# Kernel optimization log

Hardware: AMD Instinct MI355X
Metric: run time of the kernel (lower is better)

Reference implementation:

```python
import jax, jax.numpy as jnp
import numpy as np


def group_norm(x, gamma, beta, groups, eps=1e-5):
    B, C, H, W = x.shape
    xg = x.reshape(B, groups, C // groups, H, W)
    mu = xg.mean(axis=(2, 3, 4), keepdims=True)
    var = xg.var(axis=(2, 3, 4), keepdims=True)
    xn = ((xg - mu) * jax.lax.rsqrt(var + eps)).reshape(B, C, H, W)
    return xn * gamma[:, None, None] + beta[:, None, None]


def setup_inputs() -> dict:
    key = jax.random.key(0)
    ks = jax.random.split(key, 8)
    B, C, H, W = 4, 32, 256, 256
    return {
        "dec4": jax.random.normal(ks[0], (B, 512, 16, 16), jnp.float32),
        "feat": jax.random.normal(ks[1], (B, 64, H, W), jnp.float32),
        "gn_pre_gamma": jnp.ones((64,), jnp.float32),
        "gn_pre_beta": jnp.zeros((64,), jnp.float32),
        "W_pre": jax.random.normal(ks[2], (8, 64), jnp.float32) * 0.05,
        "b_pre": jnp.zeros((8,), jnp.float32),
        "gn_gap_gamma": jnp.ones((512,), jnp.float32),
        "gn_gap_beta": jnp.zeros((512,), jnp.float32),
        "W_gap": jax.random.normal(ks[3], (256, 512), jnp.float32) * 0.05,
        "b_gap": jnp.zeros((256,), jnp.float32),
        "emb": jax.random.normal(ks[4], (C, 256), jnp.float32),
        "W_ctrl": jax.random.normal(ks[5], (153, 512), jnp.float32) * 0.05,
        "b_ctrl": jnp.zeros((153,), jnp.float32),
    }


def reference(dec4, feat, gn_pre_gamma, gn_pre_beta, W_pre, b_pre,
              gn_gap_gamma, gn_gap_beta, W_gap, b_gap, emb, W_ctrl, b_ctrl):
    B = feat.shape[0]
    C = emb.shape[0]  # number of classes / dynamic-head instances
    # precls_conv: GroupNorm(16,64) -> ReLU -> 1x1 conv 64->8
    pre = jax.nn.relu(group_norm(feat, gn_pre_gamma, gn_pre_beta, 16))
    head_in = jnp.einsum('oi,bihw->bohw', W_pre, pre) + b_pre[:, None, None]  # [B,8,H,W]
    # GAP branch: GroupNorm(16,512) -> ReLU -> global avg pool -> 1x1 conv 512->256
    g = jax.nn.relu(group_norm(dec4, gn_gap_gamma, gn_gap_beta, 16)).mean(axis=(2, 3))  # [B,512]
    x_feat = g @ W_gap.T + b_gap  # [B,256]
    # controller: per (batch, class) dynamic conv params (1x1 conv == linear)
    x_cond = jnp.concatenate([
        jnp.broadcast_to(x_feat[:, None, :], (B, C, 256)),
        jnp.broadcast_to(emb[None], (B, C, 256)),
    ], axis=-1)  # [B,C,512]
    params = x_cond @ W_ctrl.T + b_ctrl  # [B,C,153]
    # split per weight_nums=[64,64,8], bias_nums=[8,8,1]
    w1 = params[..., 0:64].reshape(B, C, 8, 8)    # [out=8, in=8]
    w2 = params[..., 64:128].reshape(B, C, 8, 8)
    w3 = params[..., 128:136]                     # [out=1, in=8]
    b1 = params[..., 136:144]
    b2 = params[..., 144:152]
    b3 = params[..., 152:153]
    # batched grouped 1x1 convs (one group per (batch,class) instance)
    x1 = jax.nn.relu(jnp.einsum('bcoi,bihw->bcohw', w1, head_in) + b1[..., None, None])
    x2 = jax.nn.relu(jnp.einsum('bcoi,bcihw->bcohw', w2, x1) + b2[..., None, None])
    logits = jnp.einsum('bci,bcihw->bchw', w3, x2) + b3[..., None]  # [B,C,H,W]
    return logits
```

## Files before the change

### kernel.cpp

```cpp
#include <hip/hip_runtime.h>
#include <hip/hip_fp16.h>

typedef __fp16 h2 __attribute__((ext_vector_type(2)));

#if defined(__has_builtin)
#if __has_builtin(__builtin_amdgcn_fdot2)
#define HAVE_FDOT2 1
#endif
#endif

__device__ inline float dot2f(h2 a, h2 b, float acc) {
#ifdef HAVE_FDOT2
    return __builtin_amdgcn_fdot2(a, b, acc, false);
#else
    return acc + (float)a.x * (float)b.x + (float)a.y * (float)b.y;
#endif
}

__device__ inline float wave_sum(float v) {
#pragma unroll
    for (int off = 32; off > 0; off >>= 1) v += __shfl_down(v, off, 64);
    return v;
}

__global__ __launch_bounds__(256) void prep(
    const float* __restrict__ feat, const float* __restrict__ dec4,
    const float* __restrict__ gn_gap_gamma, const float* __restrict__ gn_gap_beta,
    const float* __restrict__ emb, const float* __restrict__ W_ctrl,
    float* __restrict__ partials, float* __restrict__ g_buf,
    float* __restrict__ E_ws) {
    int blk = blockIdx.x;
    int tid = threadIdx.x;
    int wid = tid >> 6, lane = tid & 63;
    if (blk < 512) {
        int grp = blk >> 3;
        int chunk = blk & 7;
        const float4* base = (const float4*)(feat + (size_t)grp * 262144 + (size_t)chunk * 32768);
        float sa = 0.f, qa = 0.f, sb = 0.f, qb = 0.f;
#pragma unroll 8
        for (int i = 0; i < 16; ++i) {
            float4 v = base[i * 256 + tid];
            float4 u = base[(i + 16) * 256 + tid];
            sa += v.x + v.y + v.z + v.w;
            qa += v.x * v.x + v.y * v.y + v.z * v.z + v.w * v.w;
            sb += u.x + u.y + u.z + u.w;
            qb += u.x * u.x + u.y * u.y + u.z * u.z + u.w * u.w;
        }
        __shared__ float ls[4], lq[4];
        float s = wave_sum(sa + sb);
        float q = wave_sum(qa + qb);
        if (lane == 0) { ls[wid] = s; lq[wid] = q; }
        __syncthreads();
        if (tid == 0) {
            partials[blk * 2 + 0] = ls[0] + ls[1] + ls[2] + ls[3];
            partials[blk * 2 + 1] = lq[0] + lq[1] + lq[2] + lq[3];
        }
    } else if (blk < 576) {
        int idx = blk - 512;
        int b = idx >> 4, gi = idx & 15;
        const float* base = dec4 + (size_t)idx * 8192;
        int ch = tid >> 3, sub = tid & 7;
        const float4* r = (const float4*)(base + ch * 256 + sub * 32);
        float v[32];
        float s = 0.f, q = 0.f;
#pragma unroll
        for (int i = 0; i < 8; ++i) {
            float4 a = r[i];
            v[i * 4 + 0] = a.x; v[i * 4 + 1] = a.y; v[i * 4 + 2] = a.z; v[i * 4 + 3] = a.w;
            s += a.x + a.y + a.z + a.w;
            q += a.x * a.x + a.y * a.y + a.z * a.z + a.w * a.w;
        }
        __shared__ float ls[4], lq[4], bc[2];
        s = wave_sum(s); q = wave_sum(q);
        if (lane == 0) { ls[wid] = s; lq[wid] = q; }
        __syncthreads();
        if (tid == 0) {
            float S = ls[0] + ls[1] + ls[2] + ls[3];
            float Q = lq[0] + lq[1] + lq[2] + lq[3];
            const float inv = 1.f / 8192.f;
            float mu = S * inv;
            float var = Q * inv - mu * mu;
            bc[0] = mu;
            bc[1] = rsqrtf(var + 1e-5f);
        }
        __syncthreads();
        float mu = bc[0], rs = bc[1];
        int c = gi * 32 + ch;
        float sc = rs * gn_gap_gamma[c];
        float sh = gn_gap_beta[c] - mu * sc;
        float acc = 0.f;
#pragma unroll
        for (int i = 0; i < 32; ++i) acc += fmaxf(v[i] * sc + sh, 0.f);
#pragma unroll
        for (int m = 1; m < 8; m <<= 1) acc += __shfl_xor(acc, m, 64);
        if (sub == 0) g_buf[b * 512 + c] = acc * (1.f / 256.f);
    } else {
        int c = blk - 576;
        __shared__ float es[256];
        es[tid] = emb[c * 256 + tid];
        __syncthreads();
        if (tid < 153) {
            const float4* w4 = (const float4*)(W_ctrl + tid * 512 + 256);
            const float4* e4 = (const float4*)es;
            float acc = 0.f;
#pragma unroll 8
            for (int k = 0; k < 64; ++k) {
                float4 a = w4[k], e = e4[k];
                acc += a.x * e.x + a.y * e.y + a.z * e.z + a.w * e.w;
            }
            E_ws[c * 153 + tid] = acc;
        }
    }
}

__global__ __launch_bounds__(256) void fc(
    const float* __restrict__ g_buf, const float* __restrict__ W_gap,
    const float* __restrict__ b_gap, const float* __restrict__ W_ctrl,
    const float* __restrict__ b_ctrl, const float* __restrict__ E_ws,
    unsigned char* __restrict__ pk) {
    int b = blockIdx.x, tid = threadIdx.x;
    __shared__ float gs[512];
    __shared__ float xf[256];
    __shared__ float F[160];
    gs[tid] = g_buf[b * 512 + tid];
    gs[tid + 256] = g_buf[b * 512 + 256 + tid];
    __syncthreads();
    {
        const float4* w = (const float4*)(W_gap + tid * 512);
        const float4* g4 = (const float4*)gs;
        float acc = b_gap[tid];
#pragma unroll 8
        for (int k = 0; k < 128; ++k) {
            float4 wv = w[k], gv = g4[k];
            acc += wv.x * gv.x + wv.y * gv.y + wv.z * gv.z + wv.w * gv.w;
        }
        xf[tid] = acc;
    }
    __syncthreads();
    if (tid < 160) {
        float acc = 0.f;
        if (tid < 153) {
            const float4* w = (const float4*)(W_ctrl + tid * 512);
            const float4* x4 = (const float4*)xf;
#pragma unroll 8
            for (int k = 0; k < 64; ++k) {
                float4 wv = w[k], xv = x4[k];
                acc += wv.x * xv.x + wv.y * xv.y + wv.z * xv.z + wv.w * xv.w;
            }
            acc += b_ctrl[tid];
        }
        F[tid] = acc;
    }
    __syncthreads();
    unsigned char* dst = pk + (size_t)b * 10240;
    for (int c = 0; c < 32; ++c) {
        if (tid < 152) {
            float v = F[tid] + E_ws[c * 153 + tid];
            ((__fp16*)(dst + c * 320))[tid] = (__fp16)v;
        } else if (tid == 152) {
            *(float*)(dst + c * 320 + 304) = F[152] + E_ws[c * 153 + 152];
        }
    }
}

__global__ __launch_bounds__(512, 4) void mainK(
    const float* __restrict__ feat, const float* __restrict__ partials,
    const float* __restrict__ gamma, const float* __restrict__ beta,
    const float* __restrict__ W_pre, const float* __restrict__ b_pre,
    const float4* __restrict__ pk, float* __restrict__ out) {
    int blk = blockIdx.x;
    int b = blk >> 7;
    int tid = threadIdx.x;
    int w = tid >> 6, lane = tid & 63;
    int P0 = (blk & 127) << 9;

    __shared__ __align__(16) float smem[4768];
    float4* pp   = (float4*)smem;
    float4* hi_l = (float4*)(smem + 2560);
    float* scv = smem + 4608;
    float* shv = smem + 4672;
    float* mus = smem + 4736;
    float* rss = smem + 4752;

    const float4* src = pk + (size_t)b * 640;
    for (int i = tid; i < 640; i += 512) pp[i] = src[i];

    if (tid < 16) {
        float s = 0.f, q = 0.f;
#pragma unroll
        for (int cc = 0; cc < 8; ++cc) {
            int idx = ((b * 16 + tid) * 8 + cc) * 2;
            s += partials[idx]; q += partials[idx + 1];
        }
        const float inv = 1.f / 262144.f;
        float mu = s * inv;
        float var = q * inv - mu * mu;
        mus[tid] = mu; rss[tid] = rsqrtf(var + 1e-5f);
    }
    __syncthreads();
    if (tid < 64) {
        float mu = mus[tid >> 2], rs = rss[tid >> 2];
        float sg = rs * gamma[tid];
        scv[tid] = sg;
        shv[tid] = beta[tid] - mu * sg;
    }
    __syncthreads();

    {
        float hi[8];
#pragma unroll
        for (int o = 0; o < 8; ++o) hi[o] = b_pre[o];
        const float* fb = feat + ((size_t)b << 22) + P0 + tid;
#pragma unroll
        for (int ch = 0; ch < 64; ++ch) {
            float v = fb[(size_t)ch << 16];
            float pre = fmaxf(v * scv[ch] + shv[ch], 0.f);
#pragma unroll
            for (int o = 0; o < 8; ++o) hi[o] += W_pre[o * 64 + ch] * pre;
        }
        float4 hq;
        hq.x = __builtin_bit_cast(float, __builtin_amdgcn_cvt_pkrtz(hi[0], hi[1]));
        hq.y = __builtin_bit_cast(float, __builtin_amdgcn_cvt_pkrtz(hi[2], hi[3]));
        hq.z = __builtin_bit_cast(float, __builtin_amdgcn_cvt_pkrtz(hi[4], hi[5]));
        hq.w = __builtin_bit_cast(float, __builtin_amdgcn_cvt_pkrtz(hi[6], hi[7]));
        hi_l[(tid >> 1) + (tid & 1) * 256] = hq;
    }
    __syncthreads();

    float* ob = out + ((size_t)b << 21) + P0;
#pragma unroll 1
    for (int kk = 0; kk < 4; ++kk) {
        int c = (w << 2) + kk;
        const float4* Pc = pp + c * 20;
        float4 w1r[8], w2r[8];
#pragma unroll
        for (int o = 0; o < 8; ++o) w1r[o] = Pc[o];
#pragma unroll
        for (int o = 0; o < 8; ++o) w2r[o] = Pc[8 + o];
        float4 w3r = Pc[16];
        float4 b1r = Pc[17];
        float4 b2r = Pc[18];
        float b3v = Pc[19].x;
        float b1f[8], b2f[8];
        { h2 t = __builtin_bit_cast(h2, b1r.x); b1f[0] = t.x; b1f[1] = t.y; }
        { h2 t = __builtin_bit_cast(h2, b1r.y); b1f[2] = t.x; b1f[3] = t.y; }
        { h2 t = __builtin_bit_cast(h2, b1r.z); b1f[4] = t.x; b1f[5] = t.y; }
        { h2 t = __builtin_bit_cast(h2, b1r.w); b1f[6] = t.x; b1f[7] = t.y; }
        { h2 t = __builtin_bit_cast(h2, b2r.x); b2f[0] = t.x; b2f[1] = t.y; }
        { h2 t = __builtin_bit_cast(h2, b2r.y); b2f[2] = t.x; b2f[3] = t.y; }
        { h2 t = __builtin_bit_cast(h2, b2r.z); b2f[4] = t.x; b2f[5] = t.y; }
        { h2 t = __builtin_bit_cast(h2, b2r.w); b2f[6] = t.x; b2f[7] = t.y; }

        float* cp = ob + ((size_t)c << 16);
#pragma unroll
        for (int j = 0; j < 4; ++j) {
            int q = j * 64 + lane;
            float4 ha = hi_l[q];
            float4 hb = hi_l[256 + q];
            h2 a0 = __builtin_bit_cast(h2, ha.x), a1 = __builtin_bit_cast(h2, ha.y),
               a2 = __builtin_bit_cast(h2, ha.z), a3 = __builtin_bit_cast(h2, ha.w);
            h2 e0 = __builtin_bit_cast(h2, hb.x), e1 = __builtin_bit_cast(h2, hb.y),
               e2 = __builtin_bit_cast(h2, hb.z), e3 = __builtin_bit_cast(h2, hb.w);

            float x1a[8], x1b[8];
#pragma unroll
            for (int o = 0; o < 8; ++o) {
                h2 wa = __builtin_bit_cast(h2, w1r[o].x), wb = __builtin_bit_cast(h2, w1r[o].y),
                   wc = __builtin_bit_cast(h2, w1r[o].z), wd = __builtin_bit_cast(h2, w1r[o].w);
                float s0 = dot2f(wd, a3, dot2f(wc, a2, dot2f(wb, a1, dot2f(wa, a0, b1f[o]))));
                float s1 = dot2f(wd, e3, dot2f(wc, e2, dot2f(wb, e1, dot2f(wa, e0, b1f[o]))));
                x1a[o] = fmaxf(s0, 0.f);
                x1b[o] = fmaxf(s1, 0.f);
            }
            h2 pa0 = __builtin_amdgcn_cvt_pkrtz(x1a[0], x1a[1]);
            h2 pa1 = __builtin_amdgcn_cvt_pkrtz(x1a[2], x1a[3]);
            h2 pa2 = __builtin_amdgcn_cvt_pkrtz(x1a[4], x1a[5]);
            h2 pa3 = __builtin_amdgcn_cvt_pkrtz(x1a[6], x1a[7]);
            h2 pb0 = __builtin_amdgcn_cvt_pkrtz(x1b[0], x1b[1]);
            h2 pb1 = __builtin_amdgcn_cvt_pkrtz(x1b[2], x1b[3]);
            h2 pb2 = __builtin_amdgcn_cvt_pkrtz(x1b[4], x1b[5]);
            h2 pb3 = __builtin_amdgcn_cvt_pkrtz(x1b[6], x1b[7]);

            float x2a[8], x2b[8];
#pragma unroll
            for (int o = 0; o < 8; ++o) {
                h2 wa = __builtin_bit_cast(h2, w2r[o].x), wb = __builtin_bit_cast(h2, w2r[o].y),
                   wc = __builtin_bit_cast(h2, w2r[o].z), wd = __builtin_bit_cast(h2, w2r[o].w);
                float s0 = dot2f(wd, pa3, dot2f(wc, pa2, dot2f(wb, pa1, dot2f(wa, pa0, b2f[o]))));
                float s1 = dot2f(wd, pb3, dot2f(wc, pb2, dot2f(wb, pb1, dot2f(wa, pb0, b2f[o]))));
                x2a[o] = fmaxf(s0, 0.f);
                x2b[o] = fmaxf(s1, 0.f);
            }
            h2 qa0 = __builtin_amdgcn_cvt_pkrtz(x2a[0], x2a[1]);
            h2 qa1 = __builtin_amdgcn_cvt_pkrtz(x2a[2], x2a[3]);
            h2 qa2 = __builtin_amdgcn_cvt_pkrtz(x2a[4], x2a[5]);
            h2 qa3 = __builtin_amdgcn_cvt_pkrtz(x2a[6], x2a[7]);
            h2 qb0 = __builtin_amdgcn_cvt_pkrtz(x2b[0], x2b[1]);
            h2 qb1 = __builtin_amdgcn_cvt_pkrtz(x2b[2], x2b[3]);
            h2 qb2 = __builtin_amdgcn_cvt_pkrtz(x2b[4], x2b[5]);
            h2 qb3 = __builtin_amdgcn_cvt_pkrtz(x2b[6], x2b[7]);

            h2 w3a = __builtin_bit_cast(h2, w3r.x), w3b = __builtin_bit_cast(h2, w3r.y),
               w3c = __builtin_bit_cast(h2, w3r.z), w3d = __builtin_bit_cast(h2, w3r.w);
            float lg0 = dot2f(w3d, qa3, dot2f(w3c, qa2, dot2f(w3b, qa1, dot2f(w3a, qa0, b3v))));
            float lg1 = dot2f(w3d, qb3, dot2f(w3c, qb2, dot2f(w3b, qb1, dot2f(w3a, qb0, b3v))));
            *(float2*)(cp + 2 * q) = make_float2(lg0, lg1);
        }
    }
}

extern "C" void kernel_launch(void* const* d_in, const int* in_sizes, int n_in,
                              void* d_out, int out_size, void* d_ws, size_t ws_size,
                              hipStream_t stream) {
    const float* dec4         = (const float*)d_in[0];
    const float* feat         = (const float*)d_in[1];
    const float* gn_pre_gamma = (const float*)d_in[2];
    const float* gn_pre_beta  = (const float*)d_in[3];
    const float* W_pre        = (const float*)d_in[4];
    const float* b_pre        = (const float*)d_in[5];
    const float* gn_gap_gamma = (const float*)d_in[6];
    const float* gn_gap_beta  = (const float*)d_in[7];
    const float* W_gap        = (const float*)d_in[8];
    const float* b_gap        = (const float*)d_in[9];
    const float* emb          = (const float*)d_in[10];
    const float* W_ctrl       = (const float*)d_in[11];
    const float* b_ctrl       = (const float*)d_in[12];
    float* out = (float*)d_out;
    float* ws  = (float*)d_ws;

    float* partials = ws;
    float* g_buf    = ws + 1024;
    float* E_ws     = ws + 3072;
    unsigned char* pkB = (unsigned char*)(ws + 7968);

    prep<<<608, 256, 0, stream>>>(feat, dec4, gn_gap_gamma, gn_gap_beta,
                                  emb, W_ctrl, partials, g_buf, E_ws);
    fc<<<4, 256, 0, stream>>>(g_buf, W_gap, b_gap, W_ctrl, b_ctrl, E_ws, pkB);
    mainK<<<512, 512, 0, stream>>>(feat, partials, gn_pre_gamma, gn_pre_beta,
                                   W_pre, b_pre, (const float4*)pkB, out);
}
```

Before: 90.82 us.

## Split feat stats into more blocks and vectorize dynamic-head output stores

The GroupNorm statistics pass over feat is split into 2048 smaller blocks instead of 512, giving more parallelism for the memory-bound reduction. The main kernel reorders the fp16 head_in tile in shared memory so each lane handles four consecutive pixels and writes a float4 instead of a float2. It also packs the scale and shift into a float2 and factors the 8x8 layers into helpers. The changes add more partial sums to combine per group and change the LDS access pattern.

```diff
diff --git a/kernel.cpp b/kernel.cpp
--- a/kernel.cpp
+++ b/kernel.cpp
@@ -32,15 +32,15 @@
     int blk = blockIdx.x;
     int tid = threadIdx.x;
     int wid = tid >> 6, lane = tid & 63;
-    if (blk < 512) {
-        int grp = blk >> 3;
-        int chunk = blk & 7;
-        const float4* base = (const float4*)(feat + (size_t)grp * 262144 + (size_t)chunk * 32768);
+    if (blk < 2048) {
+        int grp = blk >> 5;
+        int chunk = blk & 31;
+        const float4* base = (const float4*)(feat + (size_t)grp * 262144 + (size_t)chunk * 8192);
         float sa = 0.f, qa = 0.f, sb = 0.f, qb = 0.f;
-#pragma unroll 8
-        for (int i = 0; i < 16; ++i) {
+#pragma unroll
+        for (int i = 0; i < 4; ++i) {
             float4 v = base[i * 256 + tid];
-            float4 u = base[(i + 16) * 256 + tid];
+            float4 u = base[(i + 4) * 256 + tid];
             sa += v.x + v.y + v.z + v.w;
             qa += v.x * v.x + v.y * v.y + v.z * v.z + v.w * v.w;
             sb += u.x + u.y + u.z + u.w;
@@ -55,8 +55,8 @@
             partials[blk * 2 + 0] = ls[0] + ls[1] + ls[2] + ls[3];
             partials[blk * 2 + 1] = lq[0] + lq[1] + lq[2] + lq[3];
         }
-    } else if (blk < 576) {
-        int idx = blk - 512;
+    } else if (blk < 2112) {
+        int idx = blk - 2048;
         int b = idx >> 4, gi = idx & 15;
         const float* base = dec4 + (size_t)idx * 8192;
         int ch = tid >> 3, sub = tid & 7;
@@ -95,7 +95,7 @@
         for (int m = 1; m < 8; m <<= 1) acc += __shfl_xor(acc, m, 64);
         if (sub == 0) g_buf[b * 512 + c] = acc * (1.f / 256.f);
     } else {
-        int c = blk - 576;
+        int c = blk - 2112;
         __shared__ float es[256];
         es[tid] = emb[c * 256 + tid];
         __syncthreads();
@@ -163,6 +163,28 @@
     }
 }
 
+__device__ inline void layer8(const float4 W[8], const float bias[8],
+                              const h2 xin[4], h2 xout[4]) {
+    float t[8];
+#pragma unroll
+    for (int o = 0; o < 8; ++o) {
+        h2 wa = __builtin_bit_cast(h2, W[o].x), wb = __builtin_bit_cast(h2, W[o].y),
+           wc = __builtin_bit_cast(h2, W[o].z), wd = __builtin_bit_cast(h2, W[o].w);
+        float s = dot2f(wd, xin[3], dot2f(wc, xin[2], dot2f(wb, xin[1], dot2f(wa, xin[0], bias[o]))));
+        t[o] = fmaxf(s, 0.f);
+    }
+    xout[0] = __builtin_amdgcn_cvt_pkrtz(t[0], t[1]);
+    xout[1] = __builtin_amdgcn_cvt_pkrtz(t[2], t[3]);
+    xout[2] = __builtin_amdgcn_cvt_pkrtz(t[4], t[5]);
+    xout[3] = __builtin_amdgcn_cvt_pkrtz(t[6], t[7]);
+}
+
+__device__ inline float layer_out(float4 w3r, float b3v, const h2 z[4]) {
+    h2 wa = __builtin_bit_cast(h2, w3r.x), wb = __builtin_bit_cast(h2, w3r.y),
+       wc = __builtin_bit_cast(h2, w3r.z), wd = __builtin_bit_cast(h2, w3r.w);
+    return dot2f(wd, z[3], dot2f(wc, z[2], dot2f(wb, z[1], dot2f(wa, z[0], b3v))));
+}
+
 __global__ __launch_bounds__(512, 4) void mainK(
     const float* __restrict__ feat, const float* __restrict__ partials,
     const float* __restrict__ gamma, const float* __restrict__ beta,
@@ -177,8 +199,7 @@
     __shared__ __align__(16) float smem[4768];
     float4* pp   = (float4*)smem;
     float4* hi_l = (float4*)(smem + 2560);
-    float* scv = smem + 4608;
-    float* shv = smem + 4672;
+    float2* sch  = (float2*)(smem + 4608);
     float* mus = smem + 4736;
     float* rss = smem + 4752;
 
@@ -188,8 +209,8 @@
     if (tid < 16) {
         float s = 0.f, q = 0.f;
 #pragma unroll
-        for (int cc = 0; cc < 8; ++cc) {
-            int idx = ((b * 16 + tid) * 8 + cc) * 2;
+        for (int cc = 0; cc < 32; ++cc) {
+            int idx = ((b * 16 + tid) * 32 + cc) * 2;
             s += partials[idx]; q += partials[idx + 1];
         }
         const float inv = 1.f / 262144.f;
@@ -201,8 +222,7 @@
     if (tid < 64) {
         float mu = mus[tid >> 2], rs = rss[tid >> 2];
         float sg = rs * gamma[tid];
-        scv[tid] = sg;
-        shv[tid] = beta[tid] - mu * sg;
+        sch[tid] = make_float2(sg, beta[tid] - mu * sg);
     }
     __syncthreads();
 
@@ -214,7 +234,8 @@
 #pragma unroll
         for (int ch = 0; ch < 64; ++ch) {
             float v = fb[(size_t)ch << 16];
-            float pre = fmaxf(v * scv[ch] + shv[ch], 0.f);
+            float2 ss = sch[ch];
+            float pre = fmaxf(v * ss.x + ss.y, 0.f);
 #pragma unroll
             for (int o = 0; o < 8; ++o) hi[o] += W_pre[o * 64 + ch] * pre;
         }
@@ -223,7 +244,7 @@
         hq.y = __builtin_bit_cast(float, __builtin_amdgcn_cvt_pkrtz(hi[2], hi[3]));
         hq.z = __builtin_bit_cast(float, __builtin_amdgcn_cvt_pkrtz(hi[4], hi[5]));
         hq.w = __builtin_bit_cast(float, __builtin_amdgcn_cvt_pkrtz(hi[6], hi[7]));
-        hi_l[(tid >> 1) + (tid & 1) * 256] = hq;
+        hi_l[tid] = hq;
     }
     __syncthreads();
 
@@ -253,58 +274,40 @@
 
         float* cp = ob + ((size_t)c << 16);
 #pragma unroll
-        for (int j = 0; j < 4; ++j) {
-            int q = j * 64 + lane;
-            float4 ha = hi_l[q];
-            float4 hb = hi_l[256 + q];
-            h2 a0 = __builtin_bit_cast(h2, ha.x), a1 = __builtin_bit_cast(h2, ha.y),
-               a2 = __builtin_bit_cast(h2, ha.z), a3 = __builtin_bit_cast(h2, ha.w);
-            h2 e0 = __builtin_bit_cast(h2, hb.x), e1 = __builtin_bit_cast(h2, hb.y),
-               e2 = __builtin_bit_cast(h2, hb.z), e3 = __builtin_bit_cast(h2, hb.w);
-
-            float x1a[8], x1b[8];
-#pragma unroll
-            for (int o = 0; o < 8; ++o) {
-                h2 wa = __builtin_bit_cast(h2, w1r[o].x), wb = __builtin_bit_cast(h2, w1r[o].y),
-                   wc = __builtin_bit_cast(h2, w1r[o].z), wd = __builtin_bit_cast(h2, w1r[o].w);
-                float s0 = dot2f(wd, a3, dot2f(wc, a2, dot2f(wb, a1, dot2f(wa, a0, b1f[o]))));
-                float s1 = dot2f(wd, e3, dot2f(wc, e2, dot2f(wb, e1, dot2f(wa, e0, b1f[o]))));
-                x1a[o] = fmaxf(s0, 0.f);
-                x1b[o] = fmaxf(s1, 0.f);
+        for (int j = 0; j < 2; ++j) {
+            int pb = j * 256 + lane * 4;
+            float4 h0 = hi_l[pb + 0];
+            float4 h1 = hi_l[pb + 1];
+            float4 h2v = hi_l[pb + 2];
+            float4 h3 = hi_l[pb + 3];
+            float4 res;
+            {
+                h2 xa[4] = { __builtin_bit_cast(h2, h0.x), __builtin_bit_cast(h2, h0.y),
+                             __builtin_bit_cast(h2, h0.z), __builtin_bit_cast(h2, h0.w) };
+                h2 xb[4] = { __builtin_bit_cast(h2, h1.x), __builtin_bit_cast(h2, h1.y),
+                             __builtin_bit_cast(h2, h1.z), __builtin_bit_cast(h2, h1.w) };
+                h2 ya[4], yb[4], za[4], zb[4];
+                layer8(w1r, b1f, xa, ya);
+                layer8(w1r, b1f, xb, yb);
+                layer8(w2r, b2f, ya, za);
+                layer8(w2r, b2f, yb, zb);
+                res.x = layer_out(w3r, b3v, za);
+                res.y = layer_out(w3r, b3v, zb);
             }
-            h2 pa0 = __builtin_amdgcn_cvt_pkrtz(x1a[0], x1a[1]);
-            h2 pa1 = __builtin_amdgcn_cvt_pkrtz(x1a[2], x1a[3]);
-            h2 pa2 = __builtin_amdgcn_cvt_pkrtz(x1a[4], x1a[5]);
-            h2 pa3 = __builtin_amdgcn_cvt_pkrtz(x1a[6], x1a[7]);
-            h2 pb0 = __builtin_amdgcn_cvt_pkrtz(x1b[0], x1b[1]);
-            h2 pb1 = __builtin_amdgcn_cvt_pkrtz(x1b[2], x1b[3]);
-            h2 pb2 = __builtin_amdgcn_cvt_pkrtz(x1b[4], x1b[5]);
-            h2 pb3 = __builtin_amdgcn_cvt_pkrtz(x1b[6], x1b[7]);
-
-            float x2a[8], x2b[8];
-#pragma unroll
-            for (int o = 0; o < 8; ++o) {
-                h2 wa = __builtin_bit_cast(h2, w2r[o].x), wb = __builtin_bit_cast(h2, w2r[o].y),
-                   wc = __builtin_bit_cast(h2, w2r[o].z), wd = __builtin_bit_cast(h2, w2r[o].w);
-                float s0 = dot2f(wd, pa3, dot2f(wc, pa2, dot2f(wb, pa1, dot2f(wa, pa0, b2f[o]))));
-                float s1 = dot2f(wd, pb3, dot2f(wc, pb2, dot2f(wb, pb1, dot2f(wa, pb0, b2f[o]))));
-                x2a[o] = fmaxf(s0, 0.f);
-                x2b[o] = fmaxf(s1, 0.f);
+            {
+                h2 xa[4] = { __builtin_bit_cast(h2, h2v.x), __builtin_bit_cast(h2, h2v.y),
+                             __builtin_bit_cast(h2, h2v.z), __builtin_bit_cast(h2, h2v.w) };
+                h2 xb[4] = { __builtin_bit_cast(h2, h3.x), __builtin_bit_cast(h2, h3.y),
+                             __builtin_bit_cast(h2, h3.z), __builtin_bit_cast(h2, h3.w) };
+                h2 ya[4], yb[4], za[4], zb[4];
+                layer8(w1r, b1f, xa, ya);
+                layer8(w1r, b1f, xb, yb);
+                layer8(w2r, b2f, ya, za);
+                layer8(w2r, b2f, yb, zb);
+                res.z = layer_out(w3r, b3v, za);
+                res.w = layer_out(w3r, b3v, zb);
             }
-            h2 qa0 = __builtin_amdgcn_cvt_pkrtz(x2a[0], x2a[1]);
-            h2 qa1 = __builtin_amdgcn_cvt_pkrtz(x2a[2], x2a[3]);
-            h2 qa2 = __builtin_amdgcn_cvt_pkrtz(x2a[4], x2a[5]);
-            h2 qa3 = __builtin_amdgcn_cvt_pkrtz(x2a[6], x2a[7]);
-            h2 qb0 = __builtin_amdgcn_cvt_pkrtz(x2b[0], x2b[1]);
-            h2 qb1 = __builtin_amdgcn_cvt_pkrtz(x2b[2], x2b[3]);
-            h2 qb2 = __builtin_amdgcn_cvt_pkrtz(x2b[4], x2b[5]);
-            h2 qb3 = __builtin_amdgcn_cvt_pkrtz(x2b[6], x2b[7]);
-
-            h2 w3a = __builtin_bit_cast(h2, w3r.x), w3b = __builtin_bit_cast(h2, w3r.y),
-               w3c = __builtin_bit_cast(h2, w3r.z), w3d = __builtin_bit_cast(h2, w3r.w);
-            float lg0 = dot2f(w3d, qa3, dot2f(w3c, qa2, dot2f(w3b, qa1, dot2f(w3a, qa0, b3v))));
-            float lg1 = dot2f(w3d, qb3, dot2f(w3c, qb2, dot2f(w3b, qb1, dot2f(w3a, qb0, b3v))));
-            *(float2*)(cp + 2 * q) = make_float2(lg0, lg1);
+            *(float4*)(cp + pb) = res;
         }
     }
 }
@@ -329,12 +332,12 @@
     float* ws  = (float*)d_ws;
 
     float* partials = ws;
-    float* g_buf    = ws + 1024;
-    float* E_ws     = ws + 3072;
-    unsigned char* pkB = (unsigned char*)(ws + 7968);
-
-    prep<<<608, 256, 0, stream>>>(feat, dec4, gn_gap_gamma, gn_gap_beta,
-                                  emb, W_ctrl, partials, g_buf, E_ws);
+    float* g_buf    = ws + 4096;
+    float* E_ws     = ws + 6144;
+    unsigned char* pkB = (unsigned char*)(ws + 11040);
+
+    prep<<<2144, 256, 0, stream>>>(feat, dec4, gn_gap_gamma, gn_gap_beta,
+                                   emb, W_ctrl, partials, g_buf, E_ws);
     fc<<<4, 256, 0, stream>>>(g_buf, W_gap, b_gap, W_ctrl, b_ctrl, E_ws, pkB);
     mainK<<<512, 512, 0, stream>>>(feat, partials, gn_pre_gamma, gn_pre_beta,
                                    W_pre, b_pre, (const float4*)pkB, out);
```

Result: slower. 93.56 us (+3.0%).

## Replace per-class fdot2 dynamic convs with MFMA 16x16x16 block-diagonal matmuls

Applied to the files above, without the earlier changes.

Rewrites the dynamic-head stage of mainK so that the three per-class 1x1 convs run as MFMA f16 16x16x16 instructions instead of chains of packed fdot2. Two classes are packed block-diagonally into one 16-row A fragment, and the biases are preloaded into the accumulators. ReLU is applied on packed halves between layers. The head_in layout in shared memory changes to a plain per-thread order, and the GroupNorm scale and shift values are fused into a float2. The aim is to cut VALU instruction count, at the cost of wasted MFMA lanes from zero padding and narrow 4-byte scattered stores.

```diff
diff --git a/kernel.cpp b/kernel.cpp
--- a/kernel.cpp
+++ b/kernel.cpp
@@ -2,25 +2,30 @@
 #include <hip/hip_fp16.h>
 
 typedef __fp16 h2 __attribute__((ext_vector_type(2)));
-
+typedef __fp16 v4h __attribute__((ext_vector_type(4)));
+typedef float f32x4 __attribute__((ext_vector_type(4)));
+
+__device__ inline float wave_sum(float v) {
+#pragma unroll
+    for (int off = 32; off > 0; off >>= 1) v += __shfl_down(v, off, 64);
+    return v;
+}
+
+__device__ inline v4h relu_pack(f32x4 d) {
+    h2 lo = __builtin_amdgcn_cvt_pkrtz(d[0], d[1]);
+    h2 hi = __builtin_amdgcn_cvt_pkrtz(d[2], d[3]);
 #if defined(__has_builtin)
-#if __has_builtin(__builtin_amdgcn_fdot2)
-#define HAVE_FDOT2 1
+#if __has_builtin(__builtin_elementwise_max)
+    h2 z = {(__fp16)0, (__fp16)0};
+    lo = __builtin_elementwise_max(lo, z);
+    hi = __builtin_elementwise_max(hi, z);
+#else
+    lo.x = (__fp16)fmaxf((float)lo.x, 0.f); lo.y = (__fp16)fmaxf((float)lo.y, 0.f);
+    hi.x = (__fp16)fmaxf((float)hi.x, 0.f); hi.y = (__fp16)fmaxf((float)hi.y, 0.f);
 #endif
 #endif
-
-__device__ inline float dot2f(h2 a, h2 b, float acc) {
-#ifdef HAVE_FDOT2
-    return __builtin_amdgcn_fdot2(a, b, acc, false);
-#else
-    return acc + (float)a.x * (float)b.x + (float)a.y * (float)b.y;
-#endif
-}
-
-__device__ inline float wave_sum(float v) {
-#pragma unroll
-    for (int off = 32; off > 0; off >>= 1) v += __shfl_down(v, off, 64);
-    return v;
+    v4h r = {lo.x, lo.y, hi.x, hi.y};
+    return r;
 }
 
 __global__ __launch_bounds__(256) void prep(
@@ -163,6 +168,30 @@
     }
 }
 
+struct Frags { v4h A1, A2, A3; f32x4 C1, C2, C3; };
+
+__device__ inline Frags make_frags(const __fp16* ph, const float* smemf, int c0,
+                                   int csel, int o, int dup, int crow,
+                                   bool ok1, bool okBD) {
+    Frags f;
+    int cbA = (c0 + csel) * 160;
+    int cbB = (c0 + crow) * 160;
+    v4h z = {(__fp16)0, (__fp16)0, (__fp16)0, (__fp16)0};
+    v4h a1 = *(const v4h*)(ph + cbA + o * 8 + dup * 4);
+    v4h a2 = *(const v4h*)(ph + cbA + 64 + o * 8 + dup * 4);
+    v4h a3 = *(const v4h*)(ph + cbA + 128 + dup * 4);
+    f.A1 = ok1 ? a1 : z;
+    f.A2 = okBD ? a2 : z;
+    f.A3 = (okBD && o == 0) ? a3 : z;
+    v4h b1 = *(const v4h*)(ph + cbB + 136 + dup * 4);
+    v4h b2 = *(const v4h*)(ph + cbB + 144 + dup * 4);
+    f.C1 = f32x4{(float)b1.x, (float)b1.y, (float)b1.z, (float)b1.w};
+    f.C2 = f32x4{(float)b2.x, (float)b2.y, (float)b2.z, (float)b2.w};
+    f.C3 = f32x4{0.f, 0.f, 0.f, 0.f};
+    if (dup == 0) f.C3[0] = smemf[(c0 + crow) * 80 + 76];
+    return f;
+}
+
 __global__ __launch_bounds__(512, 4) void mainK(
     const float* __restrict__ feat, const float* __restrict__ partials,
     const float* __restrict__ gamma, const float* __restrict__ beta,
@@ -177,8 +206,7 @@
     __shared__ __align__(16) float smem[4768];
     float4* pp   = (float4*)smem;
     float4* hi_l = (float4*)(smem + 2560);
-    float* scv = smem + 4608;
-    float* shv = smem + 4672;
+    float2* sch  = (float2*)(smem + 4608);
     float* mus = smem + 4736;
     float* rss = smem + 4752;
 
@@ -201,110 +229,69 @@
     if (tid < 64) {
         float mu = mus[tid >> 2], rs = rss[tid >> 2];
         float sg = rs * gamma[tid];
-        scv[tid] = sg;
-        shv[tid] = beta[tid] - mu * sg;
+        sch[tid] = make_float2(sg, beta[tid] - mu * sg);
     }
     __syncthreads();
 
     {
         float hi[8];
 #pragma unroll
-        for (int o = 0; o < 8; ++o) hi[o] = b_pre[o];
+        for (int o2 = 0; o2 < 8; ++o2) hi[o2] = b_pre[o2];
         const float* fb = feat + ((size_t)b << 22) + P0 + tid;
 #pragma unroll
         for (int ch = 0; ch < 64; ++ch) {
             float v = fb[(size_t)ch << 16];
-            float pre = fmaxf(v * scv[ch] + shv[ch], 0.f);
-#pragma unroll
-            for (int o = 0; o < 8; ++o) hi[o] += W_pre[o * 64 + ch] * pre;
+            float2 ss = sch[ch];
+            float pre = fmaxf(v * ss.x + ss.y, 0.f);
+#pragma unroll
+            for (int o2 = 0; o2 < 8; ++o2) hi[o2] += W_pre[o2 * 64 + ch] * pre;
         }
         float4 hq;
         hq.x = __builtin_bit_cast(float, __builtin_amdgcn_cvt_pkrtz(hi[0], hi[1]));
         hq.y = __builtin_bit_cast(float, __builtin_amdgcn_cvt_pkrtz(hi[2], hi[3]));
         hq.z = __builtin_bit_cast(float, __builtin_amdgcn_cvt_pkrtz(hi[4], hi[5]));
         hq.w = __builtin_bit_cast(float, __builtin_amdgcn_cvt_pkrtz(hi[6], hi[7]));
-        hi_l[(tid >> 1) + (tid & 1) * 256] = hq;
-    }
-    __syncthreads();
+        hi_l[tid] = hq;
+    }
+    __syncthreads();
+
+    const __fp16* ph = (const __fp16*)smem;
+    int m = lane & 15;
+    int kg = lane >> 4;
+    int csel = m >> 3;
+    int o = m & 7;
+    int dup = kg & 1;
+    int crow = kg >> 1;
+    bool ok1 = (kg < 2);
+    bool okBD = (crow == csel);
+    bool act = (dup == 0);
+
+    int cA = w << 2;
+    int cB = cA + 2;
+    Frags fa = make_frags(ph, smem, cA, csel, o, dup, crow, ok1, okBD);
+    Frags fb2 = make_frags(ph, smem, cB, csel, o, dup, crow, ok1, okBD);
 
     float* ob = out + ((size_t)b << 21) + P0;
-#pragma unroll 1
-    for (int kk = 0; kk < 4; ++kk) {
-        int c = (w << 2) + kk;
-        const float4* Pc = pp + c * 20;
-        float4 w1r[8], w2r[8];
-#pragma unroll
-        for (int o = 0; o < 8; ++o) w1r[o] = Pc[o];
-#pragma unroll
-        for (int o = 0; o < 8; ++o) w2r[o] = Pc[8 + o];
-        float4 w3r = Pc[16];
-        float4 b1r = Pc[17];
-        float4 b2r = Pc[18];
-        float b3v = Pc[19].x;
-        float b1f[8], b2f[8];
-        { h2 t = __builtin_bit_cast(h2, b1r.x); b1f[0] = t.x; b1f[1] = t.y; }
-        { h2 t = __builtin_bit_cast(h2, b1r.y); b1f[2] = t.x; b1f[3] = t.y; }
-        { h2 t = __builtin_bit_cast(h2, b1r.z); b1f[4] = t.x; b1f[5] = t.y; }
-        { h2 t = __builtin_bit_cast(h2, b1r.w); b1f[6] = t.x; b1f[7] = t.y; }
-        { h2 t = __builtin_bit_cast(h2, b2r.x); b2f[0] = t.x; b2f[1] = t.y; }
-        { h2 t = __builtin_bit_cast(h2, b2r.y); b2f[2] = t.x; b2f[3] = t.y; }
-        { h2 t = __builtin_bit_cast(h2, b2r.z); b2f[4] = t.x; b2f[5] = t.y; }
-        { h2 t = __builtin_bit_cast(h2, b2r.w); b2f[6] = t.x; b2f[7] = t.y; }
-
-        float* cp = ob + ((size_t)c << 16);
-#pragma unroll
-        for (int j = 0; j < 4; ++j) {
-            int q = j * 64 + lane;
-            float4 ha = hi_l[q];
-            float4 hb = hi_l[256 + q];
-            h2 a0 = __builtin_bit_cast(h2, ha.x), a1 = __builtin_bit_cast(h2, ha.y),
-               a2 = __builtin_bit_cast(h2, ha.z), a3 = __builtin_bit_cast(h2, ha.w);
-            h2 e0 = __builtin_bit_cast(h2, hb.x), e1 = __builtin_bit_cast(h2, hb.y),
-               e2 = __builtin_bit_cast(h2, hb.z), e3 = __builtin_bit_cast(h2, hb.w);
-
-            float x1a[8], x1b[8];
-#pragma unroll
-            for (int o = 0; o < 8; ++o) {
-                h2 wa = __builtin_bit_cast(h2, w1r[o].x), wb = __builtin_bit_cast(h2, w1r[o].y),
-                   wc = __builtin_bit_cast(h2, w1r[o].z), wd = __builtin_bit_cast(h2, w1r[o].w);
-                float s0 = dot2f(wd, a3, dot2f(wc, a2, dot2f(wb, a1, dot2f(wa, a0, b1f[o]))));
-                float s1 = dot2f(wd, e3, dot2f(wc, e2, dot2f(wb, e1, dot2f(wa, e0, b1f[o]))));
-                x1a[o] = fmaxf(s0, 0.f);
-                x1b[o] = fmaxf(s1, 0.f);
-            }
-            h2 pa0 = __builtin_amdgcn_cvt_pkrtz(x1a[0], x1a[1]);
-            h2 pa1 = __builtin_amdgcn_cvt_pkrtz(x1a[2], x1a[3]);
-            h2 pa2 = __builtin_amdgcn_cvt_pkrtz(x1a[4], x1a[5]);
-            h2 pa3 = __builtin_amdgcn_cvt_pkrtz(x1a[6], x1a[7]);
-            h2 pb0 = __builtin_amdgcn_cvt_pkrtz(x1b[0], x1b[1]);
-            h2 pb1 = __builtin_amdgcn_cvt_pkrtz(x1b[2], x1b[3]);
-            h2 pb2 = __builtin_amdgcn_cvt_pkrtz(x1b[4], x1b[5]);
-            h2 pb3 = __builtin_amdgcn_cvt_pkrtz(x1b[6], x1b[7]);
-
-            float x2a[8], x2b[8];
-#pragma unroll
-            for (int o = 0; o < 8; ++o) {
-                h2 wa = __builtin_bit_cast(h2, w2r[o].x), wb = __builtin_bit_cast(h2, w2r[o].y),
-                   wc = __builtin_bit_cast(h2, w2r[o].z), wd = __builtin_bit_cast(h2, w2r[o].w);
-                float s0 = dot2f(wd, pa3, dot2f(wc, pa2, dot2f(wb, pa1, dot2f(wa, pa0, b2f[o]))));
-                float s1 = dot2f(wd, pb3, dot2f(wc, pb2, dot2f(wb, pb1, dot2f(wa, pb0, b2f[o]))));
-                x2a[o] = fmaxf(s0, 0.f);
-                x2b[o] = fmaxf(s1, 0.f);
-            }
-            h2 qa0 = __builtin_amdgcn_cvt_pkrtz(x2a[0], x2a[1]);
-            h2 qa1 = __builtin_amdgcn_cvt_pkrtz(x2a[2], x2a[3]);
-            h2 qa2 = __builtin_amdgcn_cvt_pkrtz(x2a[4], x2a[5]);
-            h2 qa3 = __builtin_amdgcn_cvt_pkrtz(x2a[6], x2a[7]);
-            h2 qb0 = __builtin_amdgcn_cvt_pkrtz(x2b[0], x2b[1]);
-            h2 qb1 = __builtin_amdgcn_cvt_pkrtz(x2b[2], x2b[3]);
-            h2 qb2 = __builtin_amdgcn_cvt_pkrtz(x2b[4], x2b[5]);
-            h2 qb3 = __builtin_amdgcn_cvt_pkrtz(x2b[6], x2b[7]);
-
-            h2 w3a = __builtin_bit_cast(h2, w3r.x), w3b = __builtin_bit_cast(h2, w3r.y),
-               w3c = __builtin_bit_cast(h2, w3r.z), w3d = __builtin_bit_cast(h2, w3r.w);
-            float lg0 = dot2f(w3d, qa3, dot2f(w3c, qa2, dot2f(w3b, qa1, dot2f(w3a, qa0, b3v))));
-            float lg1 = dot2f(w3d, qb3, dot2f(w3c, qb2, dot2f(w3b, qb1, dot2f(w3a, qb0, b3v))));
-            *(float2*)(cp + 2 * q) = make_float2(lg0, lg1);
+    float* cpA = ob + ((size_t)(cA + crow) << 16) + m;
+    float* cpB = ob + ((size_t)(cB + crow) << 16) + m;
+    const __fp16* hp = ph + 5120 + m * 8 + dup * 4;
+
+#pragma unroll 4
+    for (int g = 0; g < 32; ++g) {
+        v4h B1 = *(const v4h*)(hp + g * 128);
+        f32x4 d1a = __builtin_amdgcn_mfma_f32_16x16x16f16(fa.A1, B1, fa.C1, 0, 0, 0);
+        f32x4 d1b = __builtin_amdgcn_mfma_f32_16x16x16f16(fb2.A1, B1, fb2.C1, 0, 0, 0);
+        v4h p2a = relu_pack(d1a);
+        v4h p2b = relu_pack(d1b);
+        f32x4 d2a = __builtin_amdgcn_mfma_f32_16x16x16f16(fa.A2, p2a, fa.C2, 0, 0, 0);
+        f32x4 d2b = __builtin_amdgcn_mfma_f32_16x16x16f16(fb2.A2, p2b, fb2.C2, 0, 0, 0);
+        v4h p3a = relu_pack(d2a);
+        v4h p3b = relu_pack(d2b);
+        f32x4 d3a = __builtin_amdgcn_mfma_f32_16x16x16f16(fa.A3, p3a, fa.C3, 0, 0, 0);
+        f32x4 d3b = __builtin_amdgcn_mfma_f32_16x16x16f16(fb2.A3, p3b, fb2.C3, 0, 0, 0);
+        if (act) {
+            cpA[g * 16] = d3a[0];
+            cpB[g * 16] = d3b[0];
         }
     }
 }
```

Measured after the change: 73.32 us. 19.3% less time.
